# Performance work log

Measured on AMD Instinct MI355X. Metric: run time of the kernel, lower is better.

The kernel has to match this reference:

```python
import jax, jax.numpy as jnp
import numpy as np
import math

B, S, IN_DIM, EMBED, H = 4, 2048, 1024, 1024, 16
HD = EMBED // H

def setup_inputs() -> dict:
    key = jax.random.key(0)
    ks = jax.random.split(key, 8)
    scale = 0.02
    return {
        "q": jax.random.normal(ks[0], (B, S, IN_DIM), jnp.float32),
        "k": jax.random.normal(ks[1], (B, S, IN_DIM), jnp.float32),
        "v": jax.random.normal(ks[2], (B, S, IN_DIM), jnp.float32),
        "mask": jnp.ones((B, 1, S, S), jnp.int32),
        "Wk": jax.random.normal(ks[3], (EMBED, IN_DIM), jnp.float32) * scale,
        "bk": jnp.zeros((EMBED,), jnp.float32),
        "Wv": jax.random.normal(ks[4], (EMBED, IN_DIM), jnp.float32) * scale,
        "bv": jnp.zeros((EMBED,), jnp.float32),
        "Wo": jax.random.normal(ks[5], (IN_DIM, EMBED), jnp.float32) * scale,
        "bo": jnp.zeros((IN_DIM,), jnp.float32),
    }

def _split_heads(x):
    # [B,S,E] -> [B,H,S,HD]
    b, s, _ = x.shape
    return x.reshape(b, s, H, HD).transpose(0, 2, 1, 3)

def reference(q, k, v, mask, Wk, bk, Wv, bv, Wo, bo):
    # NOTE: faithful to the original bug: q is projected with Wv, not Wq.
    vp = _split_heads(v @ Wv.T + bv)
    kp = _split_heads(k @ Wk.T + bk)
    qp = _split_heads(q @ Wv.T + bv)
    score = jnp.einsum('bhqd,bhkd->bhqk', qp, kp) / math.sqrt(HD)
    score = jnp.where(mask == 0, -jnp.inf, score)
    attn = jax.nn.softmax(score, axis=-1)
    ctx = jnp.einsum('bhqk,bhkd->bhqd', attn, vp)
    ctx = ctx.transpose(0, 2, 1, 3).reshape(q.shape[0], q.shape[1], EMBED)
    out = ctx @ Wo.T + bo
    return (out, attn)
```

## Files before the change

### kernel.cpp

```cpp
#include <hip/hip_runtime.h>
#include <stdint.h>

typedef unsigned short u16;
typedef unsigned int u32;
typedef float f32x4 __attribute__((ext_vector_type(4)));
typedef __bf16 bf16x8 __attribute__((ext_vector_type(8)));
typedef u16 u16x8 __attribute__((ext_vector_type(8)));
typedef u16 u16x4 __attribute__((ext_vector_type(4)));

#define NB   4
#define SEQ  2048
#define EMB  1024
#define NH   16
#define HDIM 64

#define QSCALE 0.18033688011112042f

__device__ __forceinline__ f32x4 mfma16(bf16x8 a, bf16x8 b, f32x4 c) {
  return __builtin_amdgcn_mfma_f32_16x16x32_bf16(a, b, c, 0, 0, 0);
}
__device__ __forceinline__ u16 f2bf(float f) {
  u32 u = __builtin_bit_cast(u32, f);
  u += 0x7FFFu + ((u >> 16) & 1u);
  return (u16)(u >> 16);
}
__device__ __forceinline__ u32 pk2bf(float lo, float hi) {
  return (u32)f2bf(lo) | ((u32)f2bf(hi) << 16);
}
__device__ __forceinline__ float bf2f(u16 h) {
  return __builtin_bit_cast(float, (u32)h << 16);
}
__device__ __forceinline__ bf16x8 ldg8(const u16* p) {
  return *reinterpret_cast<const bf16x8*>(p);
}

__global__ __launch_bounds__(256) void prep_kernel(
    const float* __restrict__ q, const float* __restrict__ k, const float* __restrict__ v,
    const float* __restrict__ Wk, const float* __restrict__ Wv, const float* __restrict__ Wo,
    const int* __restrict__ mask,
    u16* __restrict__ qb, u16* __restrict__ kb, u16* __restrict__ vb,
    u16* __restrict__ Wkb, u16* __restrict__ Wvb, u16* __restrict__ Wob,
    u32* __restrict__ bits) {
  const int y = blockIdx.y;
  if (y == 6) {
    const int idx = blockIdx.x * 256 + threadIdx.x;
    if (idx >= NB * SEQ * 64) return;
    const int w = idx & 63;
    const size_t rowbase = (size_t)(idx >> 6) * SEQ;
    const int4* p = reinterpret_cast<const int4*>(mask + rowbase + w * 32);
    u32 m = 0;
#pragma unroll
    for (int j = 0; j < 8; ++j) {
      int4 v4 = p[j];
      m |= (v4.x != 0 ? 1u : 0u) << (j * 4 + 0);
      m |= (v4.y != 0 ? 1u : 0u) << (j * 4 + 1);
      m |= (v4.z != 0 ? 1u : 0u) << (j * 4 + 2);
      m |= (v4.w != 0 ? 1u : 0u) << (j * 4 + 3);
    }
    bits[idx] = m;
    return;
  }
  const float* src; u16* dst; int n8;
  switch (y) {
    case 0: src = q;  dst = qb;  n8 = NB * SEQ * EMB / 8; break;
    case 1: src = k;  dst = kb;  n8 = NB * SEQ * EMB / 8; break;
    case 2: src = v;  dst = vb;  n8 = NB * SEQ * EMB / 8; break;
    case 3: src = Wk; dst = Wkb; n8 = EMB * EMB / 8; break;
    case 4: src = Wv; dst = Wvb; n8 = EMB * EMB / 8; break;
    default: src = Wo; dst = Wob; n8 = EMB * EMB / 8; break;
  }
  int i = blockIdx.x * 256 + threadIdx.x;
  if (i >= n8) return;
  const float4* s = reinterpret_cast<const float4*>(src) + (size_t)i * 2;
  float4 a = s[0], b = s[1];
  u16x8 o;
  o[0] = f2bf(a.x); o[1] = f2bf(a.y); o[2] = f2bf(a.z); o[3] = f2bf(a.w);
  o[4] = f2bf(b.x); o[5] = f2bf(b.y); o[6] = f2bf(b.z); o[7] = f2bf(b.w);
  reinterpret_cast<u16x8*>(dst)[i] = o;
}

__global__ __launch_bounds__(256) void tileok_kernel(const u32* __restrict__ bits,
                                                     unsigned char* __restrict__ tok) {
  const int idx = blockIdx.x * 256 + threadIdx.x;
  const int b = idx >> 10, qt = (idx >> 5) & 31, kt = idx & 31;
  const u32* bb = bits + (size_t)b * SEQ * 64;
  u32 acc = 0xFFFFFFFFu;
  for (int rr = 0; rr < 64; ++rr) {
    const u32* pr = bb + (size_t)(qt * 64 + rr) * 64 + kt * 2;
    acc &= pr[0] & pr[1];
  }
  tok[idx] = (acc == 0xFFFFFFFFu) ? 1 : 0;
}

__device__ __forceinline__ void gemm_tile(const u16* __restrict__ A,
                                          const u16* __restrict__ W,
                                          int brow, int bcol, int tid,
                                          u16* As, u16* Bs, f32x4 acc[4][4]) {
  const int K = 1024;
  const int l = tid & 63, wv = tid >> 6;
  const int lr = l & 15, lg = l >> 4;
  const int wr = wv >> 1, wc = wv & 1;
  const int srow = l >> 3;
  const int skb = (l & 7) * 16;

  for (int k0 = 0; k0 < K; k0 += 64) {
#pragma unroll
    for (int r = 0; r < 4; ++r) {
      const int chunk = r * 4 + wv;
      const int row = chunk * 8 + srow;
      const char* ga = (const char*)A + ((size_t)(brow + row) * K + k0) * 2 + skb;
      const char* gb = (const char*)W + ((size_t)(bcol + row) * K + k0) * 2 + skb;
      __builtin_amdgcn_global_load_lds(
          (const __attribute__((address_space(1))) u32*)ga,
          (__attribute__((address_space(3))) u32*)((char*)As + chunk * 1024), 16, 0, 0);
      __builtin_amdgcn_global_load_lds(
          (const __attribute__((address_space(1))) u32*)gb,
          (__attribute__((address_space(3))) u32*)((char*)Bs + chunk * 1024), 16, 0, 0);
    }
    __syncthreads();
#pragma unroll
    for (int ks = 0; ks < 2; ++ks) {
      bf16x8 af[4], bfr[4];
#pragma unroll
      for (int m = 0; m < 4; ++m)
        af[m] = *reinterpret_cast<const bf16x8*>(
            (const char*)As + (wr * 64 + m * 16 + lr) * 128 + ks * 64 + lg * 16);
#pragma unroll
      for (int n = 0; n < 4; ++n)
        bfr[n] = *reinterpret_cast<const bf16x8*>(
            (const char*)Bs + (wc * 64 + n * 16 + lr) * 128 + ks * 64 + lg * 16);
#pragma unroll
      for (int m = 0; m < 4; ++m)
#pragma unroll
        for (int n = 0; n < 4; ++n)
          acc[m][n] = mfma16(af[m], bfr[n], acc[m][n]);
    }
    __syncthreads();
  }
}

__global__ __launch_bounds__(256) void proj_gemm(
    const u16* __restrict__ qb, const u16* __restrict__ kb, const u16* __restrict__ vb,
    const u16* __restrict__ Wvb, const u16* __restrict__ Wkb,
    const float* __restrict__ bv, const float* __restrict__ bkp,
    u16* __restrict__ qp, u16* __restrict__ kp, u16* __restrict__ vpT) {
  __shared__ __align__(16) u32 smem_u32[8192];
  u16* As = (u16*)smem_u32;
  u16* Bs = As + 128 * 64;
  const int z = blockIdx.z;
  const u16* A = (z == 0) ? qb : (z == 1) ? kb : vb;
  const u16* W = (z == 1) ? Wkb : Wvb;
  const float* bias = (z == 1) ? bkp : bv;
  const int brow = blockIdx.y * 128;
  const int bcol = blockIdx.x * 128;
  const int tid = threadIdx.x;
  f32x4 acc[4][4] = {};
  gemm_tile(A, W, brow, bcol, tid, As, Bs, acc);
  const int l = tid & 63, wv = tid >> 6;
  const int lr = l & 15, lg = l >> 4;
  const int wr = wv >> 1, wc = wv & 1;

  if (z == 2) {
#pragma unroll
    for (int m = 0; m < 4; ++m)
#pragma unroll
      for (int n = 0; n < 4; ++n) {
        const int cl = wc * 64 + n * 16 + lr;
        const float b0 = bias[bcol + cl];
        const u32 w0 = pk2bf(acc[m][n][0] + b0, acc[m][n][1] + b0);
        const u32 w1 = pk2bf(acc[m][n][2] + b0, acc[m][n][3] + b0);
        const int rp0 = wr * 32 + m * 8 + lg * 2;
        const int a32 = cl * 64 + (rp0 ^ ((lr & 7) << 2));
        uint2 wv2; wv2.x = w0; wv2.y = w1;
        *reinterpret_cast<uint2*>(&smem_u32[a32]) = wv2;
      }
    __syncthreads();
#pragma unroll
    for (int i = 0; i < 8; ++i) {
      const int idx = i * 256 + tid;
      const int cl = idx >> 4;
      const int rp0 = (idx & 15) * 4;
      const int a32 = cl * 64 + (rp0 ^ ((cl & 7) << 2));
      const uint4 d = *reinterpret_cast<const uint4*>(&smem_u32[a32]);
      const int col = bcol + cl, hh = col >> 6, hd = col & 63;
      const int row = brow + rp0 * 2, bb = row >> 11, s = row & 2047;
      *reinterpret_cast<uint4*>(
          vpT + ((((size_t)bb * NH + hh) * HDIM + hd) * SEQ + s)) = d;
    }
  } else {
    u16* dst = (z == 0) ? qp : kp;
    const float sc = (z == 0) ? QSCALE : 1.0f;
#pragma unroll
    for (int m = 0; m < 4; ++m)
#pragma unroll
      for (int n = 0; n < 4; ++n)
#pragma unroll
        for (int r = 0; r < 4; ++r) {
          const int row = brow + wr * 64 + m * 16 + lg * 4 + r;
          const int col = bcol + wc * 64 + n * 16 + lr;
          const float vl = (acc[m][n][r] + bias[col]) * sc;
          const int bb = row >> 11, s = row & 2047, hh = col >> 6, hd = col & 63;
          dst[(((size_t)bb * NH + hh) * SEQ + s) * HDIM + hd] = f2bf(vl);
        }
  }
}

__global__ __launch_bounds__(256) void out_gemm(
    const u16* __restrict__ ctxb, const u16* __restrict__ Wob,
    const float* __restrict__ bo, float* __restrict__ outF) {
  __shared__ __align__(16) u32 smem_u32[8192];
  u16* As = (u16*)smem_u32;
  u16* Bs = As + 128 * 64;
  const int brow = blockIdx.y * 128;
  const int bcol = blockIdx.x * 128;
  const int tid = threadIdx.x;
  f32x4 acc[4][4] = {};
  gemm_tile(ctxb, Wob, brow, bcol, tid, As, Bs, acc);
  const int l = tid & 63, wv = tid >> 6;
  const int lr = l & 15, lg = l >> 4;
  const int wr = wv >> 1, wc = wv & 1;
#pragma unroll
  for (int m = 0; m < 4; ++m)
#pragma unroll
    for (int n = 0; n < 4; ++n)
#pragma unroll
      for (int r = 0; r < 4; ++r) {
        const int row = brow + wr * 64 + m * 16 + lg * 4 + r;
        const int col = bcol + wc * 64 + n * 16 + lr;
        outF[(size_t)row * EMB + col] = acc[m][n][r] + bo[col];
      }
}

__global__ __launch_bounds__(256) void attn_kernel(
    const u16* __restrict__ qp, const u16* __restrict__ kp, const u16* __restrict__ vpT,
    const u32* __restrict__ bits, const unsigned char* __restrict__ tok,
    float* __restrict__ attn, u16* __restrict__ ctxb) {
  __shared__ __align__(16) u16 pbuf[4][32][64];
  __shared__ __align__(16) u16 Ks[2][4096];
  const int tid = threadIdx.x;
  const int l = tid & 63, wid = tid >> 6;
  const int lr = l & 15, lg = l >> 4;
  const int bid = blockIdx.x;
  const int swz = (bid & 7) * 128 + (bid >> 3);
  const int Wn = swz * 4 + wid;
  const int qt = Wn & 63, h = (Wn >> 6) & 15, b = Wn >> 10;
  const int q0 = qt * 32;
  const size_t bh = (size_t)b * NH + h;
  const u16* qpb = qp + bh * (SEQ * HDIM);
  const u16* kpb = kp + bh * (SEQ * HDIM);
  const u16* vpb = vpT + bh * (HDIM * SEQ);
  float* attb = attn + bh * ((size_t)SEQ * SEQ);
  const unsigned char* tokb = tok + ((size_t)b * 32 + (qt >> 1)) * 32;
  const u32* bitsb = bits + (size_t)b * SEQ * 64;

  bf16x8 aq[2][2];
#pragma unroll
  for (int g = 0; g < 2; ++g)
#pragma unroll
    for (int d = 0; d < 2; ++d)
      aq[g][d] = ldg8(qpb + (size_t)(q0 + g * 16 + lr) * HDIM + d * 32 + lg * 8);

  auto stage_k = [&](int kt, int bufi) {
#pragma unroll
    for (int c = 0; c < 2; ++c) {
      const int gi = c * 256 + tid;
      const int row = gi >> 3, cs = gi & 7;
      const int csx = cs ^ (row & 7);
      __builtin_amdgcn_global_load_lds(
          (const __attribute__((address_space(1))) u32*)
              ((const char*)(kpb + (size_t)(kt * 64 + row) * HDIM) + csx * 16),
          (__attribute__((address_space(3))) u32*)
              ((char*)&Ks[bufi][0] + c * 4096 + wid * 1024),
          16, 0, 0);
    }
  };

  float sums[2][4] = {{0.f, 0.f, 0.f, 0.f}, {0.f, 0.f, 0.f, 0.f}};
  stage_k(0, 0);
  for (int kt = 0; kt < 32; ++kt) {
    const int cur = kt & 1;
    asm volatile("s_waitcnt vmcnt(0)" ::: "memory");
    __builtin_amdgcn_sched_barrier(0);
    __builtin_amdgcn_s_barrier();
    bf16x8 bk8[4][2];
#pragma unroll
    for (int st = 0; st < 4; ++st)
#pragma unroll
      for (int d = 0; d < 2; ++d) {
        const int row = st * 16 + lr;
        bk8[st][d] = *reinterpret_cast<const bf16x8*>(
            &Ks[cur][(((row << 3) | ((d * 4 + lg) ^ (row & 7)))) << 3]);
      }
    if (kt + 1 < 32) stage_k(kt + 1, cur ^ 1);
    const int kc = kt * 64;
    const bool okt = tokb[kt] != 0;
#pragma unroll
    for (int g = 0; g < 2; ++g)
#pragma unroll
      for (int st = 0; st < 4; ++st) {
        f32x4 s = {0.f, 0.f, 0.f, 0.f};
        s = mfma16(aq[g][0], bk8[st][0], s);
        s = mfma16(aq[g][1], bk8[st][1], s);
#pragma unroll
        for (int r = 0; r < 4; ++r) {
          float sc = s[r];
          if (!okt) {
            const int qrow = q0 + g * 16 + lg * 4 + r;
            const int kpos = kc + st * 16 + lr;
            const u32 wb = bitsb[(size_t)qrow * 64 + (kpos >> 5)];
            if (!((wb >> (kpos & 31)) & 1u)) sc = -1e30f;
          }
          sums[g][r] += __builtin_amdgcn_exp2f(sc);
        }
      }
  }
  float rinv[2][4];
#pragma unroll
  for (int g = 0; g < 2; ++g)
#pragma unroll
    for (int r = 0; r < 4; ++r) {
      float vsum = sums[g][r];
      vsum += __shfl_xor(vsum, 1);
      vsum += __shfl_xor(vsum, 2);
      vsum += __shfl_xor(vsum, 4);
      vsum += __shfl_xor(vsum, 8);
      rinv[g][r] = 1.0f / vsum;
    }
  __syncthreads();

  f32x4 cacc[2][4] = {};
  for (int kt = 0; kt < 32; ++kt) {
    const int kc = kt * 64;
    const bool okt = tokb[kt] != 0;
    bf16x8 bk8[4][2];
#pragma unroll
    for (int st = 0; st < 4; ++st)
#pragma unroll
      for (int d = 0; d < 2; ++d)
        bk8[st][d] = ldg8(kpb + (size_t)(kc + st * 16 + lr) * HDIM + d * 32 + lg * 8);
#pragma unroll
    for (int g = 0; g < 2; ++g)
#pragma unroll
      for (int st = 0; st < 4; ++st) {
        f32x4 s = {0.f, 0.f, 0.f, 0.f};
        s = mfma16(aq[g][0], bk8[st][0], s);
        s = mfma16(aq[g][1], bk8[st][1], s);
#pragma unroll
        for (int r = 0; r < 4; ++r) {
          float sc = s[r];
          if (!okt) {
            const int qrow = q0 + g * 16 + lg * 4 + r;
            const int kpos = kc + st * 16 + lr;
            const u32 wb = bitsb[(size_t)qrow * 64 + (kpos >> 5)];
            if (!((wb >> (kpos & 31)) & 1u)) sc = -1e30f;
          }
          const float pn = __builtin_amdgcn_exp2f(sc) * rinv[g][r];
          const int row = g * 16 + lg * 4 + r;
          const int col = st * 16 + lr;
          pbuf[wid][row][col ^ ((row & 7) << 3)] = f2bf(pn);
        }
      }
    bf16x8 vf[4][2];
#pragma unroll
    for (int ds = 0; ds < 4; ++ds)
#pragma unroll
      for (int x = 0; x < 2; ++x)
        vf[ds][x] = ldg8(vpb + (size_t)(ds * 16 + lr) * SEQ + kc + x * 32 + lg * 8);
#pragma unroll
    for (int g = 0; g < 2; ++g)
#pragma unroll
      for (int ks = 0; ks < 2; ++ks) {
        const int prow = g * 16 + lr;
        const int cb = ks * 32 + lg * 8;
        const bf16x8 pa = *reinterpret_cast<const bf16x8*>(
            &pbuf[wid][prow][cb ^ ((prow & 7) << 3)]);
#pragma unroll
        for (int ds = 0; ds < 4; ++ds)
          cacc[g][ds] = mfma16(pa, vf[ds][ks], cacc[g][ds]);
      }
#pragma unroll
    for (int i = 0; i < 8; ++i) {
      const int row = i * 4 + lg;
      const int c4 = (l & 15) * 4;
      const u16x4 raw = *reinterpret_cast<const u16x4*>(
          &pbuf[wid][row][c4 ^ ((row & 7) << 3)]);
      f32x4 o;
      o[0] = bf2f(raw[0]); o[1] = bf2f(raw[1]);
      o[2] = bf2f(raw[2]); o[3] = bf2f(raw[3]);
      __builtin_nontemporal_store(
          o, reinterpret_cast<f32x4*>(attb + (size_t)(q0 + row) * SEQ + kc + c4));
    }
  }

#pragma unroll
  for (int g = 0; g < 2; ++g)
#pragma unroll
    for (int ds = 0; ds < 4; ++ds)
#pragma unroll
      for (int r = 0; r < 4; ++r)
        ctxb[((size_t)b * SEQ + q0 + g * 16 + lg * 4 + r) * EMB + h * HDIM + ds * 16 + lr] =
            f2bf(cacc[g][ds][r]);
}

extern "C" void kernel_launch(void* const* d_in, const int* in_sizes, int n_in,
                              void* d_out, int out_size, void* d_ws, size_t ws_size,
                              hipStream_t stream) {
  const float* q   = (const float*)d_in[0];
  const float* k   = (const float*)d_in[1];
  const float* v   = (const float*)d_in[2];
  const int* mask  = (const int*)d_in[3];
  const float* Wk  = (const float*)d_in[4];
  const float* bk  = (const float*)d_in[5];
  const float* Wv  = (const float*)d_in[6];
  const float* bv  = (const float*)d_in[7];
  const float* Wo  = (const float*)d_in[8];
  const float* bo  = (const float*)d_in[9];

  float* outF = (float*)d_out;
  float* attnF = outF + (size_t)NB * SEQ * EMB;

  const size_t MiB = 1024 * 1024;
  char* ws = (char*)d_ws;
  u16* qb   = (u16*)(ws + 0 * MiB);
  u16* kb   = (u16*)(ws + 16 * MiB);
  u16* vb   = (u16*)(ws + 32 * MiB);
  u16* Wvb  = (u16*)(ws + 48 * MiB);
  u16* Wkb  = (u16*)(ws + 50 * MiB);
  u16* Wob  = (u16*)(ws + 52 * MiB);
  u16* qpB  = (u16*)(ws + 54 * MiB);
  u16* kpB  = (u16*)(ws + 70 * MiB);
  u16* vpT  = (u16*)(ws + 86 * MiB);
  u16* ctxb = (u16*)(ws + 102 * MiB);
  u32* bits = (u32*)(ws + 118 * MiB);
  unsigned char* tok = (unsigned char*)(ws + 120 * MiB);

  prep_kernel<<<dim3(NB * SEQ * EMB / 8 / 256, 7), 256, 0, stream>>>(
      q, k, v, Wk, Wv, Wo, mask, qb, kb, vb, Wkb, Wvb, Wob, bits);

  tileok_kernel<<<NB * 32 * 32 / 256, 256, 0, stream>>>(bits, tok);

  proj_gemm<<<dim3(EMB / 128, NB * SEQ / 128, 3), 256, 0, stream>>>(
      qb, kb, vb, Wvb, Wkb, bv, bk, qpB, kpB, vpT);

  attn_kernel<<<1024, 256, 0, stream>>>(
      qpB, kpB, vpT, bits, tok, attnF, ctxb);

  out_gemm<<<dim3(EMB / 128, NB * SEQ / 128), 256, 0, stream>>>(ctxb, Wob, bo, outF);
}
```

Baseline: 479.5 us.

## Stage K and V tiles through double-buffered LDS in attention second pass

In the second attention pass, K and V tiles are now loaded cooperatively into double-buffered shared memory with async global-to-LDS copies, instead of each wave loading them straight from global memory. The four waves in a block share the same batch and head, so one staged tile serves all of them. This cuts redundant global traffic and overlaps the next tile's load with current compute. It costs 16KB more LDS per block, which may lower occupancy, plus a per-iteration barrier. It also relies on a hand-tuned vmcnt(8) wait that assumes how many stores are issued after each stage.

Measured after the change: 427.9 us, median of 2. 1.12x faster.

```diff
diff --git a/kernel.cpp b/kernel.cpp
--- a/kernel.cpp
+++ b/kernel.cpp
@@ -237,6 +237,7 @@
     float* __restrict__ attn, u16* __restrict__ ctxb) {
   __shared__ __align__(16) u16 pbuf[4][32][64];
   __shared__ __align__(16) u16 Ks[2][4096];
+  __shared__ __align__(16) u16 Vs[2][4096];
   const int tid = threadIdx.x;
   const int l = tid & 63, wid = tid >> 6;
   const int lr = l & 15, lg = l >> 4;
@@ -274,6 +275,20 @@
           16, 0, 0);
     }
   };
+  auto stage_v = [&](int kt, int bufi) {
+#pragma unroll
+    for (int c = 0; c < 2; ++c) {
+      const int gi = c * 256 + tid;
+      const int row = gi >> 3, cs = gi & 7;
+      const int csx = cs ^ (row & 7);
+      __builtin_amdgcn_global_load_lds(
+          (const __attribute__((address_space(1))) u32*)
+              ((const char*)(vpb + (size_t)row * SEQ + kt * 64) + csx * 16),
+          (__attribute__((address_space(3))) u32*)
+              ((char*)&Vs[bufi][0] + c * 4096 + wid * 1024),
+          16, 0, 0);
+    }
+  };
 
   float sums[2][4] = {{0.f, 0.f, 0.f, 0.f}, {0.f, 0.f, 0.f, 0.f}};
   stage_k(0, 0);
@@ -329,15 +344,32 @@
   __syncthreads();
 
   f32x4 cacc[2][4] = {};
+  stage_k(0, 0);
+  stage_v(0, 0);
   for (int kt = 0; kt < 32; ++kt) {
+    const int cur = kt & 1;
+    if (kt == 0) {
+      asm volatile("s_waitcnt vmcnt(0)" ::: "memory");
+    } else {
+      asm volatile("s_waitcnt vmcnt(8)" ::: "memory");
+    }
+    __builtin_amdgcn_sched_barrier(0);
+    __builtin_amdgcn_s_barrier();
+    if (kt + 1 < 32) {
+      stage_k(kt + 1, cur ^ 1);
+      stage_v(kt + 1, cur ^ 1);
+    }
+    bf16x8 bk8[4][2];
+#pragma unroll
+    for (int st = 0; st < 4; ++st)
+#pragma unroll
+      for (int d = 0; d < 2; ++d) {
+        const int row = st * 16 + lr;
+        bk8[st][d] = *reinterpret_cast<const bf16x8*>(
+            &Ks[cur][(((row << 3) | ((d * 4 + lg) ^ (row & 7)))) << 3]);
+      }
     const int kc = kt * 64;
     const bool okt = tokb[kt] != 0;
-    bf16x8 bk8[4][2];
-#pragma unroll
-    for (int st = 0; st < 4; ++st)
-#pragma unroll
-      for (int d = 0; d < 2; ++d)
-        bk8[st][d] = ldg8(kpb + (size_t)(kc + st * 16 + lr) * HDIM + d * 32 + lg * 8);
 #pragma unroll
     for (int g = 0; g < 2; ++g)
 #pragma unroll
@@ -364,8 +396,11 @@
 #pragma unroll
     for (int ds = 0; ds < 4; ++ds)
 #pragma unroll
-      for (int x = 0; x < 2; ++x)
-        vf[ds][x] = ldg8(vpb + (size_t)(ds * 16 + lr) * SEQ + kc + x * 32 + lg * 8);
+      for (int x = 0; x < 2; ++x) {
+        const int row = ds * 16 + lr;
+        vf[ds][x] = *reinterpret_cast<const bf16x8*>(
+            &Vs[cur][(((row << 3) | ((x * 4 + lg) ^ (row & 7)))) << 3]);
+      }
 #pragma unroll
     for (int g = 0; g < 2; ++g)
 #pragma unroll
```
